# Optimization experiments

Measured on AMD Instinct MI355X. Metric: run time of the kernel, lower is better.

## Reference

```python
import jax, jax.numpy as jnp
import numpy as np

N_NODES = 100000
N_EDGES = 3200000
C_FEAT = 512
F_OUT = 1


def setup_inputs() -> dict:
    key = jax.random.key(0)
    k1, k2, k3 = jax.random.split(key, 3)
    x = jax.random.normal(k1, (N_NODES, C_FEAT), dtype=jnp.float32)
    edge_index = jax.random.randint(k2, (2, N_EDGES), 0, N_NODES, dtype=jnp.int64)
    # GCNConv lin weight (glorot-ish scale) and zero-init bias, as in PyG defaults
    W = jax.random.normal(k3, (F_OUT, C_FEAT), dtype=jnp.float32) / np.sqrt(C_FEAT)
    b = jnp.zeros((F_OUT,), dtype=jnp.float32)
    return {"x": x, "edge_index": edge_index, "W": W, "b": b}


def reference(x, edge_index, W, b):
    N = x.shape[0]
    # GCNConv: project first (lin has no bias), then normalized aggregation
    h = x @ W.T  # [N, F_OUT]
    # add self-loops
    loops = jnp.arange(N, dtype=edge_index.dtype)
    row = jnp.concatenate([edge_index[0], loops])  # source
    col = jnp.concatenate([edge_index[1], loops])  # target
    # symmetric normalization: deg over targets (incl. self-loop weight 1)
    deg = jax.ops.segment_sum(jnp.ones_like(col, dtype=h.dtype), col, num_segments=N)
    dinv = jnp.where(deg > 0, jax.lax.rsqrt(deg), 0.0)
    norm = dinv[row] * dinv[col]  # [E+N]
    msg = h[row] * norm[:, None]  # gather + scale
    out = jax.ops.segment_sum(msg, col, num_segments=N) + b  # scatter-add + bias
    # F_out == 1 branch of forward
    return jax.nn.sigmoid(out)
```

## Files before the change

### kernel.cpp

```cpp
#include <hip/hip_runtime.h>
#include <hip/hip_fp16.h>
#include <math.h>

#define NN 100000
#define NE 3200000
#define CF 512

#define NPARTS  8
#define PART    12500
#define NSLICES 64
#define EPB     (NE / NSLICES)
#define NPB     (NSLICES * NPARTS)

#define OFF_H    12800000
#define OFF_G    13200000
#define OFF_DINV 13600000

__device__ __forceinline__ bool detect_f64(const int* __restrict__ e32) {
    unsigned v = ((const unsigned*)e32)[2 * (threadIdx.x & 63) + 1];
    return __ballot(v != 0u) == 0ULL;
}

__device__ __forceinline__ int4 load_col4(const int* __restrict__ e32, bool f64, int e) {
    if (f64) {
        const int4* q = (const int4*)(e32 + 2 * (NE + e));
        int4 a = q[0], b = q[1];
        return make_int4(a.x, a.z, b.x, b.z);
    }
    return *(const int4*)(e32 + NE + e);
}

__device__ __forceinline__ int4 load_row4(const int* __restrict__ e32, bool f64, int e) {
    if (f64) {
        const int4* q = (const int4*)(e32 + 2 * e);
        int4 a = q[0], b = q[1];
        return make_int4(a.x, a.z, b.x, b.z);
    }
    return *(const int4*)(e32 + e);
}

#define NODES_PER_BLK 196

__global__ __launch_bounds__(1024) void deg_h_kernel(const int* __restrict__ e32,
                                                     const float* __restrict__ x,
                                                     const float* __restrict__ W,
                                                     unsigned short* __restrict__ deg_part,
                                                     float* __restrict__ h) {
    __shared__ int hist[PART];
    int tid = threadIdx.x;
    for (int i = tid; i < PART; i += 1024) hist[i] = 0;
    __syncthreads();

    int w = tid >> 6, lane = tid & 63;
    if (w < 12) {
        bool f64 = detect_f64(e32);
        int p = blockIdx.x >> 6;
        int s = blockIdx.x & 63;
        int lo = p * PART;
        int base = s * EPB;
        for (int e = base + tid * 4; e < base + EPB; e += 3072) {
            int4 c = load_col4(e32, f64, e);
            unsigned l0 = (unsigned)(c.x - lo), l1 = (unsigned)(c.y - lo);
            unsigned l2 = (unsigned)(c.z - lo), l3 = (unsigned)(c.w - lo);
            if (l0 < PART) atomicAdd(&hist[l0], 1);
            if (l1 < PART) atomicAdd(&hist[l1], 1);
            if (l2 < PART) atomicAdd(&hist[l2], 1);
            if (l3 < PART) atomicAdd(&hist[l3], 1);
        }
    } else {
        const float4* Wr = (const float4*)W;
        float4 w0 = Wr[lane], w1 = Wr[lane + 64];
        int start = blockIdx.x * NODES_PER_BLK;
        int end = start + NODES_PER_BLK;
        for (int i = start + (w - 12) * 2; i < end; i += 8) {
            int i1 = i + 1;
            float s0 = 0.f, s1 = 0.f;
            if (i < NN) {
                const float4* xr = (const float4*)(x + (size_t)i * CF);
                float4 a = xr[lane], bq = xr[lane + 64];
                s0 = a.x * w0.x + a.y * w0.y + a.z * w0.z + a.w * w0.w
                   + bq.x * w1.x + bq.y * w1.y + bq.z * w1.z + bq.w * w1.w;
            }
            if (i1 < NN) {
                const float4* xr = (const float4*)(x + (size_t)i1 * CF);
                float4 a = xr[lane], bq = xr[lane + 64];
                s1 = a.x * w0.x + a.y * w0.y + a.z * w0.z + a.w * w0.w
                   + bq.x * w1.x + bq.y * w1.y + bq.z * w1.z + bq.w * w1.w;
            }
#pragma unroll
            for (int off = 32; off >= 1; off >>= 1) {
                s0 += __shfl_down(s0, off, 64);
                s1 += __shfl_down(s1, off, 64);
            }
            if (lane == 0) {
                if (i < NN) h[i] = s0;
                if (i1 < NN) h[i1] = s1;
            }
        }
    }
    __syncthreads();
    unsigned short* outp = deg_part + (size_t)blockIdx.x * PART;
    for (int i = tid; i < PART; i += 1024) outp[i] = (unsigned short)hist[i];
}

__global__ void dinv_g_kernel(const unsigned short* __restrict__ deg_part,
                              const float* __restrict__ h,
                              float* __restrict__ dinv,
                              float* __restrict__ g) {
    int i = blockIdx.x * blockDim.x + threadIdx.x;
    if (i >= NN) return;
    int p = i / PART, l = i - p * PART;
    const unsigned short* bp = deg_part + ((size_t)(p << 6)) * PART + l;
    int d = 1;
#pragma unroll
    for (int s = 0; s < NSLICES; ++s) d += bp[(size_t)s * PART];
    float di = rsqrtf((float)d);
    dinv[i] = di;
    g[i] = h[i] * di;
}

__global__ __launch_bounds__(1024) void scatter_lds_kernel(const int* __restrict__ e32,
                                                           const float* __restrict__ g,
                                                           __half* __restrict__ s_part) {
    __shared__ float hs[PART];
    int tid = threadIdx.x;
    for (int i = tid; i < PART; i += 1024) hs[i] = 0.f;
    __syncthreads();

    bool f64 = detect_f64(e32);
    int p = blockIdx.x >> 6;
    int s = blockIdx.x & 63;
    int lo = p * PART;
    int base = s * EPB;
    for (int e = base + tid * 4; e < base + EPB; e += 4096) {
        int4 c = load_col4(e32, f64, e);
        int4 r = load_row4(e32, f64, e);
        unsigned l0 = (unsigned)(c.x - lo), l1 = (unsigned)(c.y - lo);
        unsigned l2 = (unsigned)(c.z - lo), l3 = (unsigned)(c.w - lo);
        if (l0 < PART) atomicAdd(&hs[l0], g[r.x]);
        if (l1 < PART) atomicAdd(&hs[l1], g[r.y]);
        if (l2 < PART) atomicAdd(&hs[l2], g[r.z]);
        if (l3 < PART) atomicAdd(&hs[l3], g[r.w]);
    }
    __syncthreads();
    __half* outp = s_part + (size_t)blockIdx.x * PART;
    for (int i = tid; i < PART; i += 1024) outp[i] = __float2half(hs[i]);
}

__global__ void final_kernel(const __half* __restrict__ s_part,
                             const float* __restrict__ g,
                             const float* __restrict__ dinv,
                             const float* __restrict__ b,
                             float* __restrict__ out) {
    int i = blockIdx.x * blockDim.x + threadIdx.x;
    if (i >= NN) return;
    int p = i / PART, l = i - p * PART;
    const __half* bp = s_part + ((size_t)(p << 6)) * PART + l;
    float acc = g[i];
#pragma unroll
    for (int s = 0; s < NSLICES; ++s) acc += __half2float(bp[(size_t)s * PART]);
    float v = dinv[i] * acc + b[0];
    out[i] = 1.f / (1.f + expf(-v));
}

extern "C" void kernel_launch(void* const* d_in, const int* in_sizes, int n_in,
                              void* d_out, int out_size, void* d_ws, size_t ws_size,
                              hipStream_t stream) {
    const float* x = (const float*)d_in[0];
    const int* eidx = (const int*)d_in[1];
    const float* W = (const float*)d_in[2];
    const float* b = (const float*)d_in[3];
    float* out = (float*)d_out;

    char* ws = (char*)d_ws;
    unsigned short* part_u16 = (unsigned short*)(ws);
    __half* part_h = (__half*)(ws);
    float* h = (float*)(ws + OFF_H);
    float* g = (float*)(ws + OFF_G);
    float* dinv = (float*)(ws + OFF_DINV);

    deg_h_kernel<<<NPB, 1024, 0, stream>>>(eidx, x, W, part_u16, h);
    dinv_g_kernel<<<(NN + 255) / 256, 256, 0, stream>>>(part_u16, h, dinv, g);
    scatter_lds_kernel<<<NPB, 1024, 0, stream>>>(eidx, g, part_h);
    final_kernel<<<(NN + 255) / 256, 256, 0, stream>>>(part_h, g, dinv, b, out);
}
```

Measured before the change: 368.4 us.

## Pack degree histogram as 16-bit pairs to halve partitions and load rows lazily

The degree pass now keeps two 16-bit counters in each 32-bit LDS word. This lets each block cover 25000 nodes, so there are 4 node partitions and 128 edge slices instead of 8 and 64, and each edge column is read half as many times. The scatter kernel now loads row indices one at a time, and only for edges whose target is in the block's partition, so it skips most row-index traffic. The trade-offs are that dinv_g now sums 128 partial slices, and the workspace grows to hold the degree and scatter partials in separate regions.

Result: no change. 362.3 us (-1.7%).

```diff
diff --git a/kernel.cpp b/kernel.cpp
--- a/kernel.cpp
+++ b/kernel.cpp
@@ -6,22 +6,29 @@
 #define NE 3200000
 #define CF 512
 
+#define DNP     4
+#define DPT     25000
+#define DNSL    128
+#define DEPB    (NE / DNSL)
+#define NPB     512
+#define NODES_PER_BLK 196
+
 #define NPARTS  8
 #define PART    12500
 #define NSLICES 64
 #define EPB     (NE / NSLICES)
-#define NPB     (NSLICES * NPARTS)
 
-#define OFF_H    12800000
-#define OFF_G    13200000
-#define OFF_DINV 13600000
+#define OFF_SPART 25600000
+#define OFF_G     38400000
+#define OFF_H     38800000
+#define OFF_DINV  39200000
 
-__device__ __forceinline__ bool detect_f64(const int* __restrict__ e32) {
+__device__ __forceinline__ bool detect_f64(const int* e32) {
     unsigned v = ((const unsigned*)e32)[2 * (threadIdx.x & 63) + 1];
     return __ballot(v != 0u) == 0ULL;
 }
 
-__device__ __forceinline__ int4 load_col4(const int* __restrict__ e32, bool f64, int e) {
+__device__ __forceinline__ int4 load_col4(const int* e32, bool f64, int e) {
     if (f64) {
         const int4* q = (const int4*)(e32 + 2 * (NE + e));
         int4 a = q[0], b = q[1];
@@ -29,43 +36,34 @@
     }
     return *(const int4*)(e32 + NE + e);
 }
-
-__device__ __forceinline__ int4 load_row4(const int* __restrict__ e32, bool f64, int e) {
-    if (f64) {
-        const int4* q = (const int4*)(e32 + 2 * e);
-        int4 a = q[0], b = q[1];
-        return make_int4(a.x, a.z, b.x, b.z);
-    }
-    return *(const int4*)(e32 + e);
+__device__ __forceinline__ int load_row(const int* e32, bool f64, int e) {
+    return f64 ? e32[2 * e] : e32[e];
 }
-
-#define NODES_PER_BLK 196
 
 __global__ __launch_bounds__(1024) void deg_h_kernel(const int* __restrict__ e32,
                                                      const float* __restrict__ x,
                                                      const float* __restrict__ W,
                                                      unsigned short* __restrict__ deg_part,
                                                      float* __restrict__ h) {
-    __shared__ int hist[PART];
+    __shared__ unsigned hist[DPT / 2];
     int tid = threadIdx.x;
-    for (int i = tid; i < PART; i += 1024) hist[i] = 0;
+    for (int i = tid; i < DPT / 2; i += 1024) hist[i] = 0u;
     __syncthreads();
-
     int w = tid >> 6, lane = tid & 63;
     if (w < 12) {
         bool f64 = detect_f64(e32);
-        int p = blockIdx.x >> 6;
-        int s = blockIdx.x & 63;
-        int lo = p * PART;
-        int base = s * EPB;
-        for (int e = base + tid * 4; e < base + EPB; e += 3072) {
+        int p = blockIdx.x >> 7;
+        int s = blockIdx.x & 127;
+        unsigned lo = (unsigned)(p * DPT);
+        int base = s * DEPB;
+        for (int e = base + tid * 4; e < base + DEPB; e += 3072) {
             int4 c = load_col4(e32, f64, e);
-            unsigned l0 = (unsigned)(c.x - lo), l1 = (unsigned)(c.y - lo);
-            unsigned l2 = (unsigned)(c.z - lo), l3 = (unsigned)(c.w - lo);
-            if (l0 < PART) atomicAdd(&hist[l0], 1);
-            if (l1 < PART) atomicAdd(&hist[l1], 1);
-            if (l2 < PART) atomicAdd(&hist[l2], 1);
-            if (l3 < PART) atomicAdd(&hist[l3], 1);
+            unsigned l0 = (unsigned)c.x - lo, l1 = (unsigned)c.y - lo;
+            unsigned l2 = (unsigned)c.z - lo, l3 = (unsigned)c.w - lo;
+            if (l0 < DPT) atomicAdd(&hist[l0 >> 1], 1u << ((l0 & 1) << 4));
+            if (l1 < DPT) atomicAdd(&hist[l1 >> 1], 1u << ((l1 & 1) << 4));
+            if (l2 < DPT) atomicAdd(&hist[l2 >> 1], 1u << ((l2 & 1) << 4));
+            if (l3 < DPT) atomicAdd(&hist[l3 >> 1], 1u << ((l3 & 1) << 4));
         }
     } else {
         const float4* Wr = (const float4*)W;
@@ -99,8 +97,9 @@
         }
     }
     __syncthreads();
-    unsigned short* outp = deg_part + (size_t)blockIdx.x * PART;
-    for (int i = tid; i < PART; i += 1024) outp[i] = (unsigned short)hist[i];
+    unsigned short* outp = deg_part + (size_t)blockIdx.x * DPT;
+    for (int i = tid; i < DPT; i += 1024)
+        outp[i] = (unsigned short)((hist[i >> 1] >> ((i & 1) << 4)) & 0xffffu);
 }
 
 __global__ void dinv_g_kernel(const unsigned short* __restrict__ deg_part,
@@ -109,11 +108,11 @@
                               float* __restrict__ g) {
     int i = blockIdx.x * blockDim.x + threadIdx.x;
     if (i >= NN) return;
-    int p = i / PART, l = i - p * PART;
-    const unsigned short* bp = deg_part + ((size_t)(p << 6)) * PART + l;
-    int d = 1;
-#pragma unroll
-    for (int s = 0; s < NSLICES; ++s) d += bp[(size_t)s * PART];
+    int p = i / DPT, l = i - p * DPT;
+    const unsigned short* bp = deg_part + ((size_t)p * DNSL) * DPT + l;
+    unsigned d = 1;
+#pragma unroll 16
+    for (int s = 0; s < DNSL; ++s) d += bp[(size_t)s * DPT];
     float di = rsqrtf((float)d);
     dinv[i] = di;
     g[i] = h[i] * di;
@@ -126,7 +125,6 @@
     int tid = threadIdx.x;
     for (int i = tid; i < PART; i += 1024) hs[i] = 0.f;
     __syncthreads();
-
     bool f64 = detect_f64(e32);
     int p = blockIdx.x >> 6;
     int s = blockIdx.x & 63;
@@ -134,13 +132,12 @@
     int base = s * EPB;
     for (int e = base + tid * 4; e < base + EPB; e += 4096) {
         int4 c = load_col4(e32, f64, e);
-        int4 r = load_row4(e32, f64, e);
         unsigned l0 = (unsigned)(c.x - lo), l1 = (unsigned)(c.y - lo);
         unsigned l2 = (unsigned)(c.z - lo), l3 = (unsigned)(c.w - lo);
-        if (l0 < PART) atomicAdd(&hs[l0], g[r.x]);
-        if (l1 < PART) atomicAdd(&hs[l1], g[r.y]);
-        if (l2 < PART) atomicAdd(&hs[l2], g[r.z]);
-        if (l3 < PART) atomicAdd(&hs[l3], g[r.w]);
+        if (l0 < PART) atomicAdd(&hs[l0], g[load_row(e32, f64, e + 0)]);
+        if (l1 < PART) atomicAdd(&hs[l1], g[load_row(e32, f64, e + 1)]);
+        if (l2 < PART) atomicAdd(&hs[l2], g[load_row(e32, f64, e + 2)]);
+        if (l3 < PART) atomicAdd(&hs[l3], g[load_row(e32, f64, e + 3)]);
     }
     __syncthreads();
     __half* outp = s_part + (size_t)blockIdx.x * PART;
@@ -173,14 +170,14 @@
     float* out = (float*)d_out;
 
     char* ws = (char*)d_ws;
-    unsigned short* part_u16 = (unsigned short*)(ws);
-    __half* part_h = (__half*)(ws);
+    unsigned short* dpart = (unsigned short*)(ws);
+    __half* spart = (__half*)(ws + OFF_SPART);
+    float* g = (float*)(ws + OFF_G);
     float* h = (float*)(ws + OFF_H);
-    float* g = (float*)(ws + OFF_G);
     float* dinv = (float*)(ws + OFF_DINV);
 
-    deg_h_kernel<<<NPB, 1024, 0, stream>>>(eidx, x, W, part_u16, h);
-    dinv_g_kernel<<<(NN + 255) / 256, 256, 0, stream>>>(part_u16, h, dinv, g);
-    scatter_lds_kernel<<<NPB, 1024, 0, stream>>>(eidx, g, part_h);
-    final_kernel<<<(NN + 255) / 256, 256, 0, stream>>>(part_h, g, dinv, b, out);
+    deg_h_kernel<<<NPB, 1024, 0, stream>>>(eidx, x, W, dpart, h);
+    dinv_g_kernel<<<(NN + 255) / 256, 256, 0, stream>>>(dpart, h, dinv, g);
+    scatter_lds_kernel<<<NPB, 1024, 0, stream>>>(eidx, g, spart);
+    final_kernel<<<(NN + 255) / 256, 256, 0, stream>>>(spart, g, dinv, b, out);
 }
```
